# Performance work log

Measured on AMD Instinct MI355X. Metric: run time of the kernel, lower is better.

The kernel has to match this reference:

```python
import jax, jax.numpy as jnp
import numpy as np

IN_DIM = 128
OUT_DIM = 128
NUM_RELS = 8
N_NODES = 50000
N_EDGES = 500000


def setup_inputs() -> dict:
    key = jax.random.key(0)
    k_x, k_ei_s, k_ei_d, k_et, k_w, k_sw = jax.random.split(key, 6)
    x = jax.random.normal(k_x, (N_NODES, IN_DIM), dtype=jnp.float32)
    src = jax.random.randint(k_ei_s, (N_EDGES,), 0, N_NODES)
    dst = jax.random.randint(k_ei_d, (N_EDGES,), 0, N_NODES)
    edge_index = jnp.stack([src, dst], axis=0).astype(jnp.int64)
    edge_type = jax.random.randint(k_et, (N_EDGES,), 0, NUM_RELS).astype(jnp.int64)
    # xavier_uniform: bound = sqrt(6/(fan_in+fan_out))
    bw = float(np.sqrt(6.0 / (IN_DIM + OUT_DIM)))
    weight = jax.random.uniform(k_w, (NUM_RELS, IN_DIM, OUT_DIM), dtype=jnp.float32, minval=-bw, maxval=bw)
    self_loop_weight = jax.random.uniform(k_sw, (IN_DIM, OUT_DIM), dtype=jnp.float32, minval=-bw, maxval=bw)
    bias = jnp.zeros((OUT_DIM,), dtype=jnp.float32)
    return {
        "x": x,
        "weight": weight,
        "self_loop_weight": self_loop_weight,
        "bias": bias,
        "edge_index": edge_index,
        "edge_type": edge_type,
        "num_entities": N_NODES,
    }


def reference(x, weight, self_loop_weight, bias, edge_index, edge_type, num_entities):
    # Relation-grouped formulation of the per-edge loop:
    # transform every node under every relation once: hr[r, n, o]
    hr = jnp.einsum("nd,rdo->rno", x, weight)
    src, dst = edge_index[0], edge_index[1]
    # per-edge message = x[src] @ weight[edge_type]  == hr[edge_type, src]
    msg = hr[edge_type, src]  # [E, out]
    agg = jax.ops.segment_sum(msg, dst, num_segments=num_entities)  # scatter-add into out[dst]
    out = agg + x @ self_loop_weight + bias
    return jax.nn.relu(out)
```

## Files before the change

kernel.cpp:

```cpp
#include <hip/hip_runtime.h>

#define IN_DIM 128
#define OUT_DIM 128
#define NUM_RELS 8
#define SCAN_ELEMS 2048

typedef unsigned short u16;
typedef u16 u16x8 __attribute__((ext_vector_type(8)));
typedef u16 u16x4 __attribute__((ext_vector_type(4)));
typedef __bf16 bf16x8 __attribute__((ext_vector_type(8)));
typedef float f32x4 __attribute__((ext_vector_type(4)));

__device__ __forceinline__ u16 f2bf(float f) {
    unsigned u = __float_as_uint(f);
    u += 0x7FFF + ((u >> 16) & 1);
    return (u16)(u >> 16);
}
__device__ __forceinline__ float bf2f(u16 h) {
    return __uint_as_float((unsigned)h << 16);
}

__global__ __launch_bounds__(256) void k_prep(
    const float* __restrict__ x, const float* __restrict__ weight,
    const float* __restrict__ slw,
    u16* __restrict__ xb, u16* __restrict__ Wb, int* __restrict__ cursor,
    int N, int BA, int BB)
{
    const int b = blockIdx.x;
    const int tid = threadIdx.x;
    if (b < BA) {
        long i = ((long)b * 256 + tid) * 4;
        if (i < (long)N * 128) {
            float4 v = *(const float4*)(x + i);
            u16x4 o;
            o[0] = f2bf(v.x); o[1] = f2bf(v.y); o[2] = f2bf(v.z); o[3] = f2bf(v.w);
            *(u16x4*)(xb + i) = o;
        }
    } else if (b < BA + BB) {
        long i = ((long)(b - BA) * 256 + tid) * 4;
        if (i < 9L * 16384) {
            const float* srcp = (i < 8L * 16384) ? (weight + i) : (slw + (i - 8L * 16384));
            float4 v = *(const float4*)srcp;
            u16x4 o;
            o[0] = f2bf(v.x); o[1] = f2bf(v.y); o[2] = f2bf(v.z); o[3] = f2bf(v.w);
            *(u16x4*)(Wb + i) = o;
        }
    } else {
        int j = (b - BA - BB) * 256 + tid;
        if (j < N) cursor[j] = 0;
    }
}

__global__ __launch_bounds__(256, 2) void mfma_gemm2(
    const u16* __restrict__ xb,
    const u16* __restrict__ Wb,
    const float* __restrict__ bias,
    u16* __restrict__ hr,
    int N, int ntiles)
{
    __shared__ u16 slab[4][16 * 68];

    const int tid   = threadIdx.x;
    const int z     = blockIdx.z;
    const int wv    = tid >> 6;
    const int lane  = tid & 63;
    const int q     = lane >> 4;
    const int l     = lane & 15;
    const int mbase = (wv >> 1) * 64;
    const int cbase = (wv & 1) * 64;

    const u16* Wz = Wb + (size_t)z * 128 * 128;

    u16x8 Bf[4][4];
    #pragma unroll
    for (int nt = 0; nt < 4; ++nt) {
        const int col = cbase + nt * 16 + l;
        #pragma unroll
        for (int kc = 0; kc < 4; ++kc) {
            const int k0 = kc * 32 + q * 8;
            #pragma unroll
            for (int j = 0; j < 8; ++j)
                Bf[nt][kc][j] = Wz[(k0 + j) * 128 + col];
        }
    }

    float bv[4];
    #pragma unroll
    for (int nt = 0; nt < 4; ++nt)
        bv[nt] = (z == 8) ? bias[cbase + nt * 16 + l] : 0.f;

    u16* slabw = &slab[wv][0];

    for (int tile = blockIdx.x; tile < ntiles; tile += gridDim.x) {
        const int n0 = tile * 128;

        f32x4 acc[4][4] = {};

        #pragma unroll
        for (int kc = 0; kc < 4; ++kc) {
            const int k0 = kc * 32 + q * 8;
            u16x8 a[4];
            #pragma unroll
            for (int mt = 0; mt < 4; ++mt) {
                const int row = n0 + mbase + mt * 16 + l;
                u16x8 v = {};
                if (row < N) v = *(const u16x8*)(xb + (size_t)row * 128 + k0);
                a[mt] = v;
            }
            #pragma unroll
            for (int nt = 0; nt < 4; ++nt) {
                bf16x8 b = __builtin_bit_cast(bf16x8, Bf[nt][kc]);
                #pragma unroll
                for (int mt = 0; mt < 4; ++mt) {
                    acc[mt][nt] = __builtin_amdgcn_mfma_f32_16x16x32_bf16(
                        __builtin_bit_cast(bf16x8, a[mt]), b, acc[mt][nt], 0, 0, 0);
                }
            }
        }

        u16* hrz = hr + ((size_t)z * N) * 128;
        #pragma unroll
        for (int mt = 0; mt < 4; ++mt) {
            #pragma unroll
            for (int nt = 0; nt < 4; ++nt) {
                const int col = nt * 16 + l;
                #pragma unroll
                for (int j = 0; j < 4; ++j) {
                    slabw[(q * 4 + j) * 68 + col] = f2bf(acc[mt][nt][j] + bv[nt]);
                }
            }
            const int srow = lane >> 3;
            const int scol = (lane & 7) * 8;
            #pragma unroll
            for (int h = 0; h < 2; ++h) {
                const int r = h * 8 + srow;
                const int grow = n0 + mbase + mt * 16 + r;
                if (grow < N) {
                    u16x8 v = *(const u16x8*)&slabw[r * 68 + scol];
                    *(u16x8*)(hrz + (size_t)grow * 128 + cbase + scol) = v;
                }
            }
        }
    }
}

__global__ __launch_bounds__(256) void k_hist(
    const int* __restrict__ dst, int* __restrict__ deg, int E)
{
    int e = blockIdx.x * blockDim.x + threadIdx.x;
    if (e < E) atomicAdd(&deg[dst[e]], 1);
}

__global__ __launch_bounds__(256) void k_scan1(
    const int* __restrict__ deg, int* __restrict__ local,
    int* __restrict__ bsum, int n)
{
    __shared__ int s[256];
    const int t = threadIdx.x;
    const int base = blockIdx.x * SCAN_ELEMS + t * 8;
    int v[8];
    int sum = 0;
    #pragma unroll
    for (int j = 0; j < 8; ++j) {
        int i = base + j;
        v[j] = (i < n) ? deg[i] : 0;
        sum += v[j];
    }
    s[t] = sum;
    __syncthreads();
    #pragma unroll
    for (int off = 1; off < 256; off <<= 1) {
        int y = (t >= off) ? s[t - off] : 0;
        __syncthreads();
        s[t] += y;
        __syncthreads();
    }
    int run = s[t] - sum;
    #pragma unroll
    for (int j = 0; j < 8; ++j) {
        int i = base + j;
        if (i < n) local[i] = run;
        run += v[j];
    }
    if (t == 255) bsum[blockIdx.x] = s[255];
}

__global__ __launch_bounds__(256) void k_scan23(
    int* __restrict__ row_ptr, const int* __restrict__ bsum,
    int* __restrict__ cursor, int B, int n)
{
    __shared__ int s[256];
    const int t = threadIdx.x;
    int v = (t < B) ? bsum[t] : 0;
    s[t] = v;
    __syncthreads();
    #pragma unroll
    for (int off = 1; off < 256; off <<= 1) {
        int y = (t >= off) ? s[t - off] : 0;
        __syncthreads();
        s[t] += y;
        __syncthreads();
    }
    const int myoff = (blockIdx.x == 0) ? 0 : s[blockIdx.x - 1];
    const int total = s[255];
    const int base = blockIdx.x * SCAN_ELEMS + t * 8;
    #pragma unroll
    for (int j = 0; j < 8; ++j) {
        int i = base + j;
        if (i < n) {
            int val = row_ptr[i] + myoff;
            row_ptr[i] = val;
            cursor[i] = val;
        }
    }
    if (blockIdx.x == 0 && t == 0) row_ptr[n] = total;
}

__global__ __launch_bounds__(256) void k_fill(
    const int* __restrict__ src, const int* __restrict__ dst,
    const int* __restrict__ et, int* __restrict__ cursor,
    int* __restrict__ packed, int E)
{
    int e = blockIdx.x * blockDim.x + threadIdx.x;
    if (e >= E) return;
    int pos = atomicAdd(&cursor[dst[e]], 1);
    packed[pos] = (et[e] << 17) | src[e];
}

__global__ __launch_bounds__(256) void gather_bf16(
    const u16* __restrict__ hr,
    const u16* __restrict__ hself,
    const int* __restrict__ row_ptr, const int* __restrict__ packed,
    float* __restrict__ out, int Nn, int N)
{
    int g = blockIdx.x * 16 + (threadIdx.x >> 4);
    int lane = threadIdx.x & 15;
    if (g >= Nn) return;
    const int beg = row_ptr[g];
    const int end = row_ptr[g + 1];
    const int lo = lane * 8;

    u16x8 sv = *(const u16x8*)(hself + (size_t)g * 128 + lo);
    float a[8], b[8], c[8], d[8];
    #pragma unroll
    for (int j = 0; j < 8; ++j) { a[j] = bf2f(sv[j]); b[j] = 0.f; c[j] = 0.f; d[j] = 0.f; }

    int k = beg;
    for (; k + 8 <= end; k += 8) {
        int p0 = packed[k],     p1 = packed[k + 1], p2 = packed[k + 2], p3 = packed[k + 3];
        int p4 = packed[k + 4], p5 = packed[k + 5], p6 = packed[k + 6], p7 = packed[k + 7];
        u16x8 v0 = *(const u16x8*)(hr + ((size_t)(p0 >> 17) * N + (p0 & 0x1FFFF)) * 128 + lo);
        u16x8 v1 = *(const u16x8*)(hr + ((size_t)(p1 >> 17) * N + (p1 & 0x1FFFF)) * 128 + lo);
        u16x8 v2 = *(const u16x8*)(hr + ((size_t)(p2 >> 17) * N + (p2 & 0x1FFFF)) * 128 + lo);
        u16x8 v3 = *(const u16x8*)(hr + ((size_t)(p3 >> 17) * N + (p3 & 0x1FFFF)) * 128 + lo);
        u16x8 v4 = *(const u16x8*)(hr + ((size_t)(p4 >> 17) * N + (p4 & 0x1FFFF)) * 128 + lo);
        u16x8 v5 = *(const u16x8*)(hr + ((size_t)(p5 >> 17) * N + (p5 & 0x1FFFF)) * 128 + lo);
        u16x8 v6 = *(const u16x8*)(hr + ((size_t)(p6 >> 17) * N + (p6 & 0x1FFFF)) * 128 + lo);
        u16x8 v7 = *(const u16x8*)(hr + ((size_t)(p7 >> 17) * N + (p7 & 0x1FFFF)) * 128 + lo);
        #pragma unroll
        for (int j = 0; j < 8; ++j) {
            a[j] += bf2f(v0[j]); b[j] += bf2f(v1[j]);
            c[j] += bf2f(v2[j]); d[j] += bf2f(v3[j]);
            a[j] += bf2f(v4[j]); b[j] += bf2f(v5[j]);
            c[j] += bf2f(v6[j]); d[j] += bf2f(v7[j]);
        }
    }
    for (; k + 4 <= end; k += 4) {
        int p0 = packed[k], p1 = packed[k + 1], p2 = packed[k + 2], p3 = packed[k + 3];
        u16x8 v0 = *(const u16x8*)(hr + ((size_t)(p0 >> 17) * N + (p0 & 0x1FFFF)) * 128 + lo);
        u16x8 v1 = *(const u16x8*)(hr + ((size_t)(p1 >> 17) * N + (p1 & 0x1FFFF)) * 128 + lo);
        u16x8 v2 = *(const u16x8*)(hr + ((size_t)(p2 >> 17) * N + (p2 & 0x1FFFF)) * 128 + lo);
        u16x8 v3 = *(const u16x8*)(hr + ((size_t)(p3 >> 17) * N + (p3 & 0x1FFFF)) * 128 + lo);
        #pragma unroll
        for (int j = 0; j < 8; ++j) {
            a[j] += bf2f(v0[j]); b[j] += bf2f(v1[j]);
            c[j] += bf2f(v2[j]); d[j] += bf2f(v3[j]);
        }
    }
    for (; k < end; ++k) {
        int p = packed[k];
        u16x8 v = *(const u16x8*)(hr + ((size_t)(p >> 17) * N + (p & 0x1FFFF)) * 128 + lo);
        #pragma unroll
        for (int j = 0; j < 8; ++j) a[j] += bf2f(v[j]);
    }
    #pragma unroll
    for (int j = 0; j < 8; ++j) a[j] = fmaxf(a[j] + b[j] + c[j] + d[j], 0.f);

    float* op = out + (size_t)g * 128 + lo;
    *(float4*)op       = make_float4(a[0], a[1], a[2], a[3]);
    *(float4*)(op + 4) = make_float4(a[4], a[5], a[6], a[7]);
}

__global__ __launch_bounds__(256) void gemm128(
    const float* __restrict__ x, const float* __restrict__ W,
    const float* __restrict__ bias, float* __restrict__ out, int N)
{
    __shared__ float Ws[IN_DIM * OUT_DIM];
    __shared__ float xs[16][IN_DIM];

    const float* Wz = W + (size_t)blockIdx.z * IN_DIM * OUT_DIM;
    float* outz = out + (size_t)blockIdx.z * (size_t)N * OUT_DIM;

    {
        const float4* s4 = (const float4*)Wz;
        float4* d4 = (float4*)Ws;
        for (int i = threadIdx.x; i < IN_DIM * OUT_DIM / 4; i += 256)
            d4[i] = s4[i];
    }

    const int tid = threadIdx.x;
    const int nl = (tid >> 5) * 2;
    const int og = (tid & 31) * 4;

    float4 b4 = make_float4(0.f, 0.f, 0.f, 0.f);
    if (bias) b4 = *(const float4*)&bias[og];

    const int nchunks = (N + 15) / 16;
    for (int chunk = blockIdx.x; chunk < nchunks; chunk += gridDim.x) {
        const int n0 = chunk * 16;
        const int rows = min(16, N - n0);
        __syncthreads();
        {
            const float4* xsrc = (const float4*)(x + (size_t)n0 * IN_DIM);
            float4* xdst = (float4*)&xs[0][0];
            const int n4 = rows * (IN_DIM / 4);
            for (int i = tid; i < n4; i += 256) xdst[i] = xsrc[i];
        }
        __syncthreads();

        if (nl < rows) {
            float a00 = 0.f, a01 = 0.f, a02 = 0.f, a03 = 0.f;
            float a10 = 0.f, a11 = 0.f, a12 = 0.f, a13 = 0.f;
            #pragma unroll 8
            for (int d = 0; d < IN_DIM; ++d) {
                const float4 w4 = *(const float4*)&Ws[d * OUT_DIM + og];
                const float xa = xs[nl][d];
                const float xb = xs[nl + 1][d];
                a00 += xa * w4.x; a01 += xa * w4.y; a02 += xa * w4.z; a03 += xa * w4.w;
                a10 += xb * w4.x; a11 += xb * w4.y; a12 += xb * w4.z; a13 += xb * w4.w;
            }
            float4 r0 = make_float4(a00 + b4.x, a01 + b4.y, a02 + b4.z, a03 + b4.w);
            *(float4*)&outz[(size_t)(n0 + nl) * OUT_DIM + og] = r0;
            if (nl + 1 < rows) {
                float4 r1 = make_float4(a10 + b4.x, a11 + b4.y, a12 + b4.z, a13 + b4.w);
                *(float4*)&outz[(size_t)(n0 + nl + 1) * OUT_DIM + og] = r1;
            }
        }
    }
}

__global__ __launch_bounds__(256) void edge_direct(
    const float* __restrict__ x, const float* __restrict__ W,
    const int* __restrict__ src, const int* __restrict__ dst,
    const int* __restrict__ et, float* __restrict__ out, int E)
{
    long t = (long)blockIdx.x * blockDim.x + threadIdx.x;
    long e = t >> 6;
    int lane = (int)(t & 63);
    if (e >= E) return;
    int s = src[e], d = dst[e], r = et[e];
    const float* xr = x + (long)s * IN_DIM;
    float2 xv = *(const float2*)(xr + lane * 2);
    const float* Wr = W + (long)r * IN_DIM * OUT_DIM;
    const int o0 = lane * 2;
    float a0 = 0.f, a1 = 0.f;
    #pragma unroll 8
    for (int dd = 0; dd < 64; ++dd) {
        float xa = __shfl(xv.x, dd);
        float xb = __shfl(xv.y, dd);
        a0 += xa * Wr[(2 * dd) * OUT_DIM + o0]     + xb * Wr[(2 * dd + 1) * OUT_DIM + o0];
        a1 += xa * Wr[(2 * dd) * OUT_DIM + o0 + 1] + xb * Wr[(2 * dd + 1) * OUT_DIM + o0 + 1];
    }
    atomicAdd(out + (long)d * OUT_DIM + o0, a0);
    atomicAdd(out + (long)d * OUT_DIM + o0 + 1, a1);
}

__global__ __launch_bounds__(256) void relu_k(float* __restrict__ out, long n4)
{
    long i = (long)blockIdx.x * blockDim.x + threadIdx.x;
    if (i >= n4) return;
    float4 v = ((float4*)out)[i];
    v.x = fmaxf(v.x, 0.f); v.y = fmaxf(v.y, 0.f);
    v.z = fmaxf(v.z, 0.f); v.w = fmaxf(v.w, 0.f);
    ((float4*)out)[i] = v;
}

static inline size_t align256(size_t x) { return (x + 255) & ~(size_t)255; }

extern "C" void kernel_launch(void* const* d_in, const int* in_sizes, int n_in,
                              void* d_out, int out_size, void* d_ws, size_t ws_size,
                              hipStream_t stream)
{
    const float* x      = (const float*)d_in[0];
    const float* weight = (const float*)d_in[1];
    const float* slw    = (const float*)d_in[2];
    const float* bias   = (const float*)d_in[3];
    const int*   ei     = (const int*)d_in[4];
    const int*   et     = (const int*)d_in[5];

    const int N = in_sizes[0] / IN_DIM;
    const int E = in_sizes[5];
    const int* src  = ei;
    const int* dstp = ei + E;

    float* out = (float*)d_out;

    size_t off = 0;
    const size_t xb_off   = off; off += align256((size_t)N * 128 * 2);
    const size_t wb_off   = off; off += align256((size_t)9 * 128 * 128 * 2);
    const size_t hr_off   = off; off += align256((size_t)9 * N * 128 * 2);
    const size_t rp_off   = off; off += align256((size_t)(N + 1) * 4);
    const size_t cur_off  = off; off += align256((size_t)N * 4);
    const size_t pk_off   = off; off += align256((size_t)E * 4);
    const size_t bs_off   = off; off += align256(256 * 4);
    const size_t need_bf16 = off;

    const int scanB = (N + SCAN_ELEMS - 1) / SCAN_ELEMS;

    if (ws_size >= need_bf16 && N <= (1 << 17) && scanB <= 256) {
        char* base   = (char*)d_ws;
        u16* xb      = (u16*)(base + xb_off);
        u16* Wb      = (u16*)(base + wb_off);
        u16* hr      = (u16*)(base + hr_off);
        int* row_ptr = (int*)(base + rp_off);
        int* cursor  = (int*)(base + cur_off);
        int* packed  = (int*)(base + pk_off);
        int* bsum    = (int*)(base + bs_off);

        const int BA = (int)(((long)N * 128 / 4 + 255) / 256);
        const int BB = (9 * 16384 / 4 + 255) / 256;
        const int BC = (N + 255) / 256;
        k_prep<<<dim3(BA + BB + BC), 256, 0, stream>>>(
            x, weight, slw, xb, Wb, cursor, N, BA, BB);

        const int ntiles = (N + 127) / 128;
        const int gx = ntiles < 56 ? ntiles : 56;
        mfma_gemm2<<<dim3(gx, 1, 9), 256, 0, stream>>>(xb, Wb, bias, hr, N, ntiles);

        k_hist<<<dim3((E + 255) / 256), 256, 0, stream>>>(dstp, cursor, E);
        k_scan1<<<dim3(scanB), 256, 0, stream>>>(cursor, row_ptr, bsum, N);
        k_scan23<<<dim3(scanB), 256, 0, stream>>>(row_ptr, bsum, cursor, scanB, N);
        k_fill<<<dim3((E + 255) / 256), 256, 0, stream>>>(src, dstp, et, cursor, packed, E);

        gather_bf16<<<dim3((N + 15) / 16), 256, 0, stream>>>(
            hr, hr + (size_t)8 * N * 128, row_ptr, packed, out, N, N);
    } else if (ws_size >= (size_t)NUM_RELS * N * 128 * 4) {
        gemm128<<<dim3(512, 1, 1), 256, 0, stream>>>(x, slw, bias, out, N);
        long nt = (long)E * 64;
        edge_direct<<<dim3((nt + 255) / 256), 256, 0, stream>>>(x, weight, src, dstp, et, out, E);
        long n4 = (long)N * OUT_DIM / 4;
        relu_k<<<dim3((n4 + 255) / 256), 256, 0, stream>>>(out, n4);
    } else {
        gemm128<<<dim3(512, 1, 1), 256, 0, stream>>>(x, slw, bias, out, N);
        long nt = (long)E * 64;
        edge_direct<<<dim3((nt + 255) / 256), 256, 0, stream>>>(x, weight, src, dstp, et, out, E);
        long n4 = (long)N * OUT_DIM / 4;
        relu_k<<<dim3((n4 + 255) / 256), 256, 0, stream>>>(out, n4);
    }
}
```

Baseline: 212.2 us.

## Aggregate raw features per relation first, then apply one fused K=1152 GEMM

Instead of transforming every node under all 9 weight matrices and gathering transformed rows, edges are bucketed by (dst, relation) and raw bf16 source features are summed per relation into shared memory. A single MFMA GEMM over the concatenated [8 relations + self] x 128 K dimension against a transposed weight then produces the output, with bias and ReLU fused in. This removes the 9x N x 128 intermediate write and read and the separate GEMM kernel. In exchange the scan runs over 8N buckets, the per-relation aggregates are rounded to bf16 before the GEMM, and each block holds a large LDS tile (about 148 KB), which limits occupancy.

Result: slower. 268.5 us (+26.6%).

```diff
diff --git a/kernel.cpp b/kernel.cpp
--- a/kernel.cpp
+++ b/kernel.cpp
@@ -23,8 +23,8 @@
 __global__ __launch_bounds__(256) void k_prep(
     const float* __restrict__ x, const float* __restrict__ weight,
     const float* __restrict__ slw,
-    u16* __restrict__ xb, u16* __restrict__ Wb, int* __restrict__ cursor,
-    int N, int BA, int BB)
+    u16* __restrict__ xb, u16* __restrict__ WbT, int* __restrict__ cursor,
+    int N, int n8, int BA, int BB)
 {
     const int b = blockIdx.x;
     const int tid = threadIdx.x;
@@ -37,118 +37,33 @@
             *(u16x4*)(xb + i) = o;
         }
     } else if (b < BA + BB) {
-        long i = ((long)(b - BA) * 256 + tid) * 4;
-        if (i < 9L * 16384) {
-            const float* srcp = (i < 8L * 16384) ? (weight + i) : (slw + (i - 8L * 16384));
-            float4 v = *(const float4*)srcp;
+        int i = ((b - BA) * 256 + tid) * 4;
+        if (i < 128 * 1152) {
+            const int col = i / 1152;
+            const int kk  = i - col * 1152;
             u16x4 o;
-            o[0] = f2bf(v.x); o[1] = f2bf(v.y); o[2] = f2bf(v.z); o[3] = f2bf(v.w);
-            *(u16x4*)(Wb + i) = o;
+            #pragma unroll
+            for (int j = 0; j < 4; ++j) {
+                const int kj = kk + j;
+                const float f = (kj < 1024)
+                    ? weight[((kj >> 7) << 14) + ((kj & 127) << 7) + col]
+                    : slw[((kj - 1024) << 7) + col];
+                o[j] = f2bf(f);
+            }
+            *(u16x4*)(WbT + i) = o;
         }
     } else {
-        int j = (b - BA - BB) * 256 + tid;
-        if (j < N) cursor[j] = 0;
-    }
-}
-
-__global__ __launch_bounds__(256, 2) void mfma_gemm2(
-    const u16* __restrict__ xb,
-    const u16* __restrict__ Wb,
-    const float* __restrict__ bias,
-    u16* __restrict__ hr,
-    int N, int ntiles)
-{
-    __shared__ u16 slab[4][16 * 68];
-
-    const int tid   = threadIdx.x;
-    const int z     = blockIdx.z;
-    const int wv    = tid >> 6;
-    const int lane  = tid & 63;
-    const int q     = lane >> 4;
-    const int l     = lane & 15;
-    const int mbase = (wv >> 1) * 64;
-    const int cbase = (wv & 1) * 64;
-
-    const u16* Wz = Wb + (size_t)z * 128 * 128;
-
-    u16x8 Bf[4][4];
-    #pragma unroll
-    for (int nt = 0; nt < 4; ++nt) {
-        const int col = cbase + nt * 16 + l;
-        #pragma unroll
-        for (int kc = 0; kc < 4; ++kc) {
-            const int k0 = kc * 32 + q * 8;
-            #pragma unroll
-            for (int j = 0; j < 8; ++j)
-                Bf[nt][kc][j] = Wz[(k0 + j) * 128 + col];
-        }
-    }
-
-    float bv[4];
-    #pragma unroll
-    for (int nt = 0; nt < 4; ++nt)
-        bv[nt] = (z == 8) ? bias[cbase + nt * 16 + l] : 0.f;
-
-    u16* slabw = &slab[wv][0];
-
-    for (int tile = blockIdx.x; tile < ntiles; tile += gridDim.x) {
-        const int n0 = tile * 128;
-
-        f32x4 acc[4][4] = {};
-
-        #pragma unroll
-        for (int kc = 0; kc < 4; ++kc) {
-            const int k0 = kc * 32 + q * 8;
-            u16x8 a[4];
-            #pragma unroll
-            for (int mt = 0; mt < 4; ++mt) {
-                const int row = n0 + mbase + mt * 16 + l;
-                u16x8 v = {};
-                if (row < N) v = *(const u16x8*)(xb + (size_t)row * 128 + k0);
-                a[mt] = v;
-            }
-            #pragma unroll
-            for (int nt = 0; nt < 4; ++nt) {
-                bf16x8 b = __builtin_bit_cast(bf16x8, Bf[nt][kc]);
-                #pragma unroll
-                for (int mt = 0; mt < 4; ++mt) {
-                    acc[mt][nt] = __builtin_amdgcn_mfma_f32_16x16x32_bf16(
-                        __builtin_bit_cast(bf16x8, a[mt]), b, acc[mt][nt], 0, 0, 0);
-                }
-            }
-        }
-
-        u16* hrz = hr + ((size_t)z * N) * 128;
-        #pragma unroll
-        for (int mt = 0; mt < 4; ++mt) {
-            #pragma unroll
-            for (int nt = 0; nt < 4; ++nt) {
-                const int col = nt * 16 + l;
-                #pragma unroll
-                for (int j = 0; j < 4; ++j) {
-                    slabw[(q * 4 + j) * 68 + col] = f2bf(acc[mt][nt][j] + bv[nt]);
-                }
-            }
-            const int srow = lane >> 3;
-            const int scol = (lane & 7) * 8;
-            #pragma unroll
-            for (int h = 0; h < 2; ++h) {
-                const int r = h * 8 + srow;
-                const int grow = n0 + mbase + mt * 16 + r;
-                if (grow < N) {
-                    u16x8 v = *(const u16x8*)&slabw[r * 68 + scol];
-                    *(u16x8*)(hrz + (size_t)grow * 128 + cbase + scol) = v;
-                }
-            }
-        }
+        int i = ((b - BA - BB) * 256 + tid) * 4;
+        if (i < n8) *(int4*)(cursor + i) = make_int4(0, 0, 0, 0);
     }
 }
 
 __global__ __launch_bounds__(256) void k_hist(
-    const int* __restrict__ dst, int* __restrict__ deg, int E)
+    const int* __restrict__ dst, const int* __restrict__ et,
+    int* __restrict__ deg, int E)
 {
     int e = blockIdx.x * blockDim.x + threadIdx.x;
-    if (e < E) atomicAdd(&deg[dst[e]], 1);
+    if (e < E) atomicAdd(&deg[(dst[e] << 3) + et[e]], 1);
 }
 
 __global__ __launch_bounds__(256) void k_scan1(
@@ -223,72 +138,118 @@
 {
     int e = blockIdx.x * blockDim.x + threadIdx.x;
     if (e >= E) return;
-    int pos = atomicAdd(&cursor[dst[e]], 1);
+    int pos = atomicAdd(&cursor[(dst[e] << 3) + et[e]], 1);
     packed[pos] = (et[e] << 17) | src[e];
 }
 
-__global__ __launch_bounds__(256) void gather_bf16(
-    const u16* __restrict__ hr,
-    const u16* __restrict__ hself,
-    const int* __restrict__ row_ptr, const int* __restrict__ packed,
-    float* __restrict__ out, int Nn, int N)
-{
-    int g = blockIdx.x * 16 + (threadIdx.x >> 4);
-    int lane = threadIdx.x & 15;
-    if (g >= Nn) return;
-    const int beg = row_ptr[g];
-    const int end = row_ptr[g + 1];
-    const int lo = lane * 8;
-
-    u16x8 sv = *(const u16x8*)(hself + (size_t)g * 128 + lo);
-    float a[8], b[8], c[8], d[8];
-    #pragma unroll
-    for (int j = 0; j < 8; ++j) { a[j] = bf2f(sv[j]); b[j] = 0.f; c[j] = 0.f; d[j] = 0.f; }
-
-    int k = beg;
-    for (; k + 8 <= end; k += 8) {
-        int p0 = packed[k],     p1 = packed[k + 1], p2 = packed[k + 2], p3 = packed[k + 3];
-        int p4 = packed[k + 4], p5 = packed[k + 5], p6 = packed[k + 6], p7 = packed[k + 7];
-        u16x8 v0 = *(const u16x8*)(hr + ((size_t)(p0 >> 17) * N + (p0 & 0x1FFFF)) * 128 + lo);
-        u16x8 v1 = *(const u16x8*)(hr + ((size_t)(p1 >> 17) * N + (p1 & 0x1FFFF)) * 128 + lo);
-        u16x8 v2 = *(const u16x8*)(hr + ((size_t)(p2 >> 17) * N + (p2 & 0x1FFFF)) * 128 + lo);
-        u16x8 v3 = *(const u16x8*)(hr + ((size_t)(p3 >> 17) * N + (p3 & 0x1FFFF)) * 128 + lo);
-        u16x8 v4 = *(const u16x8*)(hr + ((size_t)(p4 >> 17) * N + (p4 & 0x1FFFF)) * 128 + lo);
-        u16x8 v5 = *(const u16x8*)(hr + ((size_t)(p5 >> 17) * N + (p5 & 0x1FFFF)) * 128 + lo);
-        u16x8 v6 = *(const u16x8*)(hr + ((size_t)(p6 >> 17) * N + (p6 & 0x1FFFF)) * 128 + lo);
-        u16x8 v7 = *(const u16x8*)(hr + ((size_t)(p7 >> 17) * N + (p7 & 0x1FFFF)) * 128 + lo);
+#define NPB 64
+#define LDK 1160
+
+__global__ __launch_bounds__(256) void fused_rgcn(
+    const u16* __restrict__ xb,
+    const u16* __restrict__ WbT,
+    const float* __restrict__ bias,
+    const int* __restrict__ row_ptr,
+    const int* __restrict__ packed,
+    float* __restrict__ out, int N)
+{
+    __shared__ u16 agg[NPB][LDK];
+
+    const int tid = threadIdx.x;
+    const int n0 = blockIdx.x * NPB;
+
+    {
+        const int grp = tid >> 4;
+        const int lo  = (tid & 15) * 8;
+
+        for (int i = 0; i < 4; ++i) {
+            const int nl = (grp << 2) + i;
+            const int gn = n0 + nl;
+            if (gn >= N) break;
+            const int beg = row_ptr[gn << 3];
+            const int end = row_ptr[(gn << 3) + 8];
+            u16* arow = &agg[nl][0];
+            float a0=0.f,a1=0.f,a2=0.f,a3=0.f,a4=0.f,a5=0.f,a6=0.f,a7=0.f;
+            int cur = 0;
+
+#define FLUSH_() { u16x8 o_; \
+    o_[0]=f2bf(a0); o_[1]=f2bf(a1); o_[2]=f2bf(a2); o_[3]=f2bf(a3); \
+    o_[4]=f2bf(a4); o_[5]=f2bf(a5); o_[6]=f2bf(a6); o_[7]=f2bf(a7); \
+    *(u16x8*)(arow + (cur << 7) + lo) = o_; \
+    a0=0.f;a1=0.f;a2=0.f;a3=0.f;a4=0.f;a5=0.f;a6=0.f;a7=0.f; }
+
+#define PROC_(p_, v_) { const int r_ = (p_) >> 17; \
+    while (cur < r_) { FLUSH_(); ++cur; } \
+    a0 += bf2f((v_)[0]); a1 += bf2f((v_)[1]); a2 += bf2f((v_)[2]); a3 += bf2f((v_)[3]); \
+    a4 += bf2f((v_)[4]); a5 += bf2f((v_)[5]); a6 += bf2f((v_)[6]); a7 += bf2f((v_)[7]); }
+
+            int k = beg;
+            for (; k + 4 <= end; k += 4) {
+                const int p0 = packed[k],     p1 = packed[k + 1];
+                const int p2 = packed[k + 2], p3 = packed[k + 3];
+                const u16x8 v0 = *(const u16x8*)(xb + (size_t)(p0 & 0x1FFFF) * 128 + lo);
+                const u16x8 v1 = *(const u16x8*)(xb + (size_t)(p1 & 0x1FFFF) * 128 + lo);
+                const u16x8 v2 = *(const u16x8*)(xb + (size_t)(p2 & 0x1FFFF) * 128 + lo);
+                const u16x8 v3 = *(const u16x8*)(xb + (size_t)(p3 & 0x1FFFF) * 128 + lo);
+                PROC_(p0, v0); PROC_(p1, v1); PROC_(p2, v2); PROC_(p3, v3);
+            }
+            for (; k < end; ++k) {
+                const int p = packed[k];
+                const u16x8 v = *(const u16x8*)(xb + (size_t)(p & 0x1FFFF) * 128 + lo);
+                PROC_(p, v);
+            }
+            while (cur < 8) { FLUSH_(); ++cur; }
+            const u16x8 sv = *(const u16x8*)(xb + (size_t)gn * 128 + lo);
+            *(u16x8*)(arow + 1024 + lo) = sv;
+#undef PROC_
+#undef FLUSH_
+        }
+    }
+    __syncthreads();
+
+    const int wv = tid >> 6, lane = tid & 63;
+    const int q = lane >> 4, l = lane & 15;
+    const int cbase = wv << 5;
+    const float bv0 = bias[cbase + l];
+    const float bv1 = bias[cbase + 16 + l];
+
+    f32x4 acc[4][2] = {};
+
+    const u16* B0p = WbT + (size_t)(cbase + l) * 1152 + (q << 3);
+    const u16* B1p = B0p + (size_t)16 * 1152;
+
+    #pragma unroll 4
+    for (int kk = 0; kk < 36; ++kk) {
+        const int k0 = (kk << 5) + (q << 3);
+        const bf16x8 b0 = __builtin_bit_cast(bf16x8, *(const u16x8*)(B0p + (kk << 5)));
+        const bf16x8 b1 = __builtin_bit_cast(bf16x8, *(const u16x8*)(B1p + (kk << 5)));
+        const bf16x8 a0 = __builtin_bit_cast(bf16x8, *(const u16x8*)(&agg[l][k0]));
+        const bf16x8 a1 = __builtin_bit_cast(bf16x8, *(const u16x8*)(&agg[16 + l][k0]));
+        const bf16x8 a2 = __builtin_bit_cast(bf16x8, *(const u16x8*)(&agg[32 + l][k0]));
+        const bf16x8 a3 = __builtin_bit_cast(bf16x8, *(const u16x8*)(&agg[48 + l][k0]));
+        acc[0][0] = __builtin_amdgcn_mfma_f32_16x16x32_bf16(a0, b0, acc[0][0], 0, 0, 0);
+        acc[0][1] = __builtin_amdgcn_mfma_f32_16x16x32_bf16(a0, b1, acc[0][1], 0, 0, 0);
+        acc[1][0] = __builtin_amdgcn_mfma_f32_16x16x32_bf16(a1, b0, acc[1][0], 0, 0, 0);
+        acc[1][1] = __builtin_amdgcn_mfma_f32_16x16x32_bf16(a1, b1, acc[1][1], 0, 0, 0);
+        acc[2][0] = __builtin_amdgcn_mfma_f32_16x16x32_bf16(a2, b0, acc[2][0], 0, 0, 0);
+        acc[2][1] = __builtin_amdgcn_mfma_f32_16x16x32_bf16(a2, b1, acc[2][1], 0, 0, 0);
+        acc[3][0] = __builtin_amdgcn_mfma_f32_16x16x32_bf16(a3, b0, acc[3][0], 0, 0, 0);
+        acc[3][1] = __builtin_amdgcn_mfma_f32_16x16x32_bf16(a3, b1, acc[3][1], 0, 0, 0);
+    }
+
+    const int rbase = n0 + (q << 2);
+    #pragma unroll
+    for (int mt = 0; mt < 4; ++mt) {
+        const int row = rbase + (mt << 4);
         #pragma unroll
-        for (int j = 0; j < 8; ++j) {
-            a[j] += bf2f(v0[j]); b[j] += bf2f(v1[j]);
-            c[j] += bf2f(v2[j]); d[j] += bf2f(v3[j]);
-            a[j] += bf2f(v4[j]); b[j] += bf2f(v5[j]);
-            c[j] += bf2f(v6[j]); d[j] += bf2f(v7[j]);
-        }
-    }
-    for (; k + 4 <= end; k += 4) {
-        int p0 = packed[k], p1 = packed[k + 1], p2 = packed[k + 2], p3 = packed[k + 3];
-        u16x8 v0 = *(const u16x8*)(hr + ((size_t)(p0 >> 17) * N + (p0 & 0x1FFFF)) * 128 + lo);
-        u16x8 v1 = *(const u16x8*)(hr + ((size_t)(p1 >> 17) * N + (p1 & 0x1FFFF)) * 128 + lo);
-        u16x8 v2 = *(const u16x8*)(hr + ((size_t)(p2 >> 17) * N + (p2 & 0x1FFFF)) * 128 + lo);
-        u16x8 v3 = *(const u16x8*)(hr + ((size_t)(p3 >> 17) * N + (p3 & 0x1FFFF)) * 128 + lo);
-        #pragma unroll
-        for (int j = 0; j < 8; ++j) {
-            a[j] += bf2f(v0[j]); b[j] += bf2f(v1[j]);
-            c[j] += bf2f(v2[j]); d[j] += bf2f(v3[j]);
-        }
-    }
-    for (; k < end; ++k) {
-        int p = packed[k];
-        u16x8 v = *(const u16x8*)(hr + ((size_t)(p >> 17) * N + (p & 0x1FFFF)) * 128 + lo);
-        #pragma unroll
-        for (int j = 0; j < 8; ++j) a[j] += bf2f(v[j]);
-    }
-    #pragma unroll
-    for (int j = 0; j < 8; ++j) a[j] = fmaxf(a[j] + b[j] + c[j] + d[j], 0.f);
-
-    float* op = out + (size_t)g * 128 + lo;
-    *(float4*)op       = make_float4(a[0], a[1], a[2], a[3]);
-    *(float4*)(op + 4) = make_float4(a[4], a[5], a[6], a[7]);
+        for (int j = 0; j < 4; ++j) {
+            if (row + j < N) {
+                float* op = out + (size_t)(row + j) * 128 + cbase + l;
+                op[0]  = fmaxf(acc[mt][0][j] + bv0, 0.f);
+                op[16] = fmaxf(acc[mt][1][j] + bv1, 0.f);
+            }
+        }
+    }
 }
 
 __global__ __launch_bounds__(256) void gemm128(
@@ -405,45 +366,41 @@
 
     float* out = (float*)d_out;
 
+    const int n8 = N * 8;
+
     size_t off = 0;
     const size_t xb_off   = off; off += align256((size_t)N * 128 * 2);
-    const size_t wb_off   = off; off += align256((size_t)9 * 128 * 128 * 2);
-    const size_t hr_off   = off; off += align256((size_t)9 * N * 128 * 2);
-    const size_t rp_off   = off; off += align256((size_t)(N + 1) * 4);
-    const size_t cur_off  = off; off += align256((size_t)N * 4);
+    const size_t wb_off   = off; off += align256((size_t)128 * 1152 * 2);
+    const size_t rp_off   = off; off += align256((size_t)(n8 + 1) * 4);
+    const size_t cur_off  = off; off += align256((size_t)n8 * 4);
     const size_t pk_off   = off; off += align256((size_t)E * 4);
     const size_t bs_off   = off; off += align256(256 * 4);
     const size_t need_bf16 = off;
 
-    const int scanB = (N + SCAN_ELEMS - 1) / SCAN_ELEMS;
+    const int scanB = (n8 + SCAN_ELEMS - 1) / SCAN_ELEMS;
 
     if (ws_size >= need_bf16 && N <= (1 << 17) && scanB <= 256) {
         char* base   = (char*)d_ws;
         u16* xb      = (u16*)(base + xb_off);
-        u16* Wb      = (u16*)(base + wb_off);
-        u16* hr      = (u16*)(base + hr_off);
+        u16* WbT     = (u16*)(base + wb_off);
         int* row_ptr = (int*)(base + rp_off);
         int* cursor  = (int*)(base + cur_off);
         int* packed  = (int*)(base + pk_off);
         int* bsum    = (int*)(base + bs_off);
 
         const int BA = (int)(((long)N * 128 / 4 + 255) / 256);
-        const int BB = (9 * 16384 / 4 + 255) / 256;
-        const int BC = (N + 255) / 256;
+        const int BB = (128 * 1152 / 4 + 255) / 256;
+        const int BC = (n8 / 4 + 255) / 256;
         k_prep<<<dim3(BA + BB + BC), 256, 0, stream>>>(
-            x, weight, slw, xb, Wb, cursor, N, BA, BB);
-
-        const int ntiles = (N + 127) / 128;
-        const int gx = ntiles < 56 ? ntiles : 56;
-        mfma_gemm2<<<dim3(gx, 1, 9), 256, 0, stream>>>(xb, Wb, bias, hr, N, ntiles);
-
-        k_hist<<<dim3((E + 255) / 256), 256, 0, stream>>>(dstp, cursor, E);
-        k_scan1<<<dim3(scanB), 256, 0, stream>>>(cursor, row_ptr, bsum, N);
-        k_scan23<<<dim3(scanB), 256, 0, stream>>>(row_ptr, bsum, cursor, scanB, N);
+            x, weight, slw, xb, WbT, cursor, N, n8, BA, BB);
+
+        k_hist<<<dim3((E + 255) / 256), 256, 0, stream>>>(dstp, et, cursor, E);
+        k_scan1<<<dim3(scanB), 256, 0, stream>>>(cursor, row_ptr, bsum, n8);
+        k_scan23<<<dim3(scanB), 256, 0, stream>>>(row_ptr, bsum, cursor, scanB, n8);
         k_fill<<<dim3((E + 255) / 256), 256, 0, stream>>>(src, dstp, et, cursor, packed, E);
 
-        gather_bf16<<<dim3((N + 15) / 16), 256, 0, stream>>>(
-            hr, hr + (size_t)8 * N * 128, row_ptr, packed, out, N, N);
+        fused_rgcn<<<dim3((N + NPB - 1) / NPB), 256, 0, stream>>>(
+            xb, WbT, bias, row_ptr, packed, out, N);
     } else if (ws_size >= (size_t)NUM_RELS * N * 128 * 4) {
         gemm128<<<dim3(512, 1, 1), 256, 0, stream>>>(x, slw, bias, out, N);
         long nt = (long)E * 64;
```
